# Kernel tuning notes

Measured on AMD Instinct MI355X. Metric: run time of the kernel, lower is better.

Reference implementation:

```python
import jax, jax.numpy as jnp
import numpy as np

TGT, BSZ, E, H = 2048, 4, 1024, 16
HD = E // H


def setup_inputs() -> dict:
    key = jax.random.key(0)
    ks = jax.random.split(key, 9)
    s = 1.0 / np.sqrt(E)
    return {
        "query": jax.random.normal(ks[0], (TGT, BSZ, E), jnp.float32),
        "wq": jax.random.normal(ks[1], (E, E), jnp.float32) * s,
        "bq": jax.random.normal(ks[2], (E,), jnp.float32) * 0.01,
        "wk": jax.random.normal(ks[3], (E, E), jnp.float32) * s,
        "bk": jax.random.normal(ks[4], (E,), jnp.float32) * 0.01,
        "wv": jax.random.normal(ks[5], (E, E), jnp.float32) * s,
        "bv": jax.random.normal(ks[6], (E,), jnp.float32) * 0.01,
        "wo": jax.random.normal(ks[7], (E, E), jnp.float32) * s,
        "bo": jax.random.normal(ks[8], (E,), jnp.float32) * 0.01,
    }


def reference(query, wq, bq, wk, bk, wv, bv, wo, bo):
    tgt_len, bsz, embed_dim = query.shape
    scaling = HD ** (-0.5)
    # self-attention: q,k,v all projected from query (torch Linear: x @ W.T + b)
    q = (query @ wq.T + bq) * scaling
    k = query @ wk.T + bk
    v = query @ wv.T + bv
    # [T, B, E] -> [B, H, T, HD]
    def split_heads(x):
        return x.reshape(tgt_len, bsz, H, HD).transpose(1, 2, 0, 3)
    qh, kh, vh = split_heads(q), split_heads(k), split_heads(v)
    # attention scores [B, H, Tq, Tk]
    scores = jnp.einsum("bhqd,bhkd->bhqk", qh, kh)
    attn = jax.nn.softmax(scores, axis=-1)
    ctx = jnp.einsum("bhqk,bhkd->bhqd", attn, vh)  # [B, H, T, HD]
    ctx = ctx.transpose(2, 0, 1, 3).reshape(tgt_len, bsz, embed_dim)
    out = ctx @ wo.T + bo
    # need_weights=True default: average attn weights over heads [B, Tq, Tk]
    avg_attn = attn.mean(axis=1)
    return out, avg_attn
```

## Files before the change

### kernel.cpp

```cpp
#include <hip/hip_runtime.h>
#include <cstdint>
#include <cstddef>

typedef _Float16 f16;
typedef f16   f16x4 __attribute__((ext_vector_type(4)));
typedef f16   f16x8 __attribute__((ext_vector_type(8)));
typedef float f32x4 __attribute__((ext_vector_type(4)));

#define MFMA16x32(a, b, c) __builtin_amdgcn_mfma_f32_16x16x32_f16((a), (b), (c), 0, 0, 0)
#define MFMA16x16(a, b, c) __builtin_amdgcn_mfma_f32_16x16x16f16((a), (b), (c), 0, 0, 0)

__device__ __forceinline__ void gload_lds16(const void* g, void* l) {
    __builtin_amdgcn_global_load_lds(
        (const __attribute__((address_space(1))) unsigned int*)g,
        (__attribute__((address_space(3))) unsigned int*)l, 16, 0, 0);
}

__global__ void cvt_f32_f16(const float* __restrict__ in, f16* __restrict__ out, int n8) {
    int i = blockIdx.x * blockDim.x + threadIdx.x;
    if (i >= n8) return;
    const float4 a = ((const float4*)in)[i * 2];
    const float4 b = ((const float4*)in)[i * 2 + 1];
    f16x8 o;
    o[0] = (f16)a.x; o[1] = (f16)a.y; o[2] = (f16)a.z; o[3] = (f16)a.w;
    o[4] = (f16)b.x; o[5] = (f16)b.y; o[6] = (f16)b.z; o[7] = (f16)b.w;
    *(f16x8*)(out + (size_t)i * 8) = o;
}

__global__ __launch_bounds__(256, 3)
void gemm_qkv(const f16* __restrict__ A, const f16* __restrict__ B,
              const float* __restrict__ bq, const float* __restrict__ bk,
              const float* __restrict__ bv,
              f16* __restrict__ q_sp, f16* __restrict__ k_sp, f16* __restrict__ v_sp)
{
    __shared__ f16 Al[128 * 32];
    __shared__ f16 Bl[128 * 32];
    const int tid = threadIdx.x, lane = tid & 63, w = tid >> 6;
    const int wm = w >> 1, wn = w & 1;
    const int m0 = blockIdx.y * 128, n0 = blockIdx.x * 128;
    const int l15 = lane & 15, lh = lane >> 4;

    f32x4 acc[4][4] = {};

    const int c0 = w, c1 = w + 4;
    const int srow0 = c0 * 16 + (lane >> 2);
    const int srow1 = c1 * 16 + (lane >> 2);
    const int scol = (lane & 3) * 8;

    for (int k0 = 0; k0 < 1024; k0 += 32) {
        gload_lds16(A + (size_t)(m0 + srow0) * 1024 + k0 + scol, &Al[c0 * 512]);
        gload_lds16(A + (size_t)(m0 + srow1) * 1024 + k0 + scol, &Al[c1 * 512]);
        gload_lds16(B + (size_t)(n0 + srow0) * 1024 + k0 + scol, &Bl[c0 * 512]);
        gload_lds16(B + (size_t)(n0 + srow1) * 1024 + k0 + scol, &Bl[c1 * 512]);
        __syncthreads();
        f16x8 af[4], bf[4];
        #pragma unroll
        for (int i = 0; i < 4; ++i) {
            af[i] = *(const f16x8*)&Al[(wm * 64 + i * 16 + l15) * 32 + lh * 8];
            bf[i] = *(const f16x8*)&Bl[(wn * 64 + i * 16 + l15) * 32 + lh * 8];
        }
        #pragma unroll
        for (int i = 0; i < 4; ++i)
            #pragma unroll
            for (int j = 0; j < 4; ++j)
                acc[i][j] = MFMA16x32(af[i], bf[j], acc[i][j]);
        __syncthreads();
    }

    const int seg = n0 >> 10;
    const float* bias = (seg == 0) ? bq : (seg == 1) ? bk : bv;
    f16* dst = (seg == 0) ? q_sp : (seg == 1) ? k_sp : v_sp;
    const float scale = (seg == 0) ? 0.18033688011112042f : 1.0f;

    #pragma unroll
    for (int j = 0; j < 4; ++j) {
        const int n = n0 + wn * 64 + j * 16 + l15;
        const int e = n & 1023, hh = e >> 6, d = e & 63;
        const float bsv = bias[e];
        #pragma unroll
        for (int i = 0; i < 4; ++i) {
            #pragma unroll
            for (int r = 0; r < 4; ++r) {
                const int m = m0 + wm * 64 + i * 16 + lh * 4 + r;
                const int t = m >> 2, bb = m & 3;
                dst[((size_t)(bb * 16 + hh) * 2048 + t) * 64 + d] =
                    (f16)((acc[i][j][r] + bsv) * scale);
            }
        }
    }
}

__global__ __launch_bounds__(256)
void vpack(const f16* __restrict__ v_sp, f16* __restrict__ vf_) {
    __shared__ f16 L[16 * 64];
    const int nt = blockIdx.x, bh = blockIdx.y;
    const int tid = threadIdx.x;
    const f16* src = v_sp + ((size_t)bh * 2048 + nt * 16) * 64;
    if (tid < 128)
        *(f16x8*)&L[tid * 8] = *(const f16x8*)&src[tid * 8];
    __syncthreads();
    const int lane = tid >> 2, dt = tid & 3;
    const int l15 = lane & 15, lh = lane >> 4;
    f16x4 o;
    #pragma unroll
    for (int r = 0; r < 4; ++r) o[r] = L[(lh * 4 + r) * 64 + dt * 16 + l15];
    *(f16x4*)&vf_[((size_t)bh * 128 + nt) * 1024 + tid * 4] = o;
}

__global__ __launch_bounds__(512, 1)
void attn_kernel(const f16* __restrict__ q_s, const f16* __restrict__ k_s,
                 const f16* __restrict__ v_f, f16* __restrict__ ctx,
                 float* __restrict__ avg_out)
{
    __shared__ float Oacc[2][2][1024];
    __shared__ float sumL[8][2][16];

    const int tid = threadIdx.x;
    const int lane = tid & 63;
    const int w = tid >> 6;
    const int b = blockIdx.y;
    const int t0 = blockIdx.x * 32;
    const int l15 = lane & 15, lh = lane >> 4;

    f16x4 avgv0[16] = {}, avgv1[16] = {};

    {
        float* Oz = &Oacc[0][0][0];
        #pragma unroll
        for (int jj = 0; jj < 8; ++jj) Oz[tid + jj * 512] = 0.f;
    }
    __syncthreads();

    for (int h = 0; h < 16; ++h) {
        const f16* Qh  = q_s + ((size_t)(b * 16 + h) * 2048 + t0) * 64;
        const f16* Kh  = k_s + (size_t)(b * 16 + h) * 2048 * 64 + (size_t)w * 256 * 64;
        const f16* Vfh = v_f + (size_t)(b * 16 + h) * 131072 + (size_t)w * 16 * 1024;

        const f16x8 qa0 = *(const f16x8*)(Qh + l15 * 64 + lh * 8);
        const f16x8 qa1 = *(const f16x8*)(Qh + l15 * 64 + 32 + lh * 8);
        const f16x8 qb0 = *(const f16x8*)(Qh + (16 + l15) * 64 + lh * 8);
        const f16x8 qb1 = *(const f16x8*)(Qh + (16 + l15) * 64 + 32 + lh * 8);

        f16x4 tA[16], tB[16];
        float rsA = 0.f, rsB = 0.f;
        #pragma unroll
        for (int nt = 0; nt < 16; ++nt) {
            const f16* kp = Kh + (size_t)(nt * 16 + l15) * 64 + lh * 8;
            const f16x8 kf0 = *(const f16x8*)(kp);
            const f16x8 kf1 = *(const f16x8*)(kp + 32);
            f32x4 sA = {0.f, 0.f, 0.f, 0.f}, sB = {0.f, 0.f, 0.f, 0.f};
            sA = MFMA16x32(kf0, qa0, sA); sA = MFMA16x32(kf1, qa1, sA);
            sB = MFMA16x32(kf0, qb0, sB); sB = MFMA16x32(kf1, qb1, sB);
            f16x4 ta, tb;
            #pragma unroll
            for (int r = 0; r < 4; ++r) {
                const float eA = __builtin_amdgcn_exp2f(sA[r]);
                const float eB = __builtin_amdgcn_exp2f(sB[r]);
                rsA += eA; rsB += eB;
                ta[r] = (f16)eA; tb[r] = (f16)eB;
            }
            tA[nt] = ta; tB[nt] = tb;
        }
        rsA += __shfl_xor(rsA, 16); rsA += __shfl_xor(rsA, 32);
        rsB += __shfl_xor(rsB, 16); rsB += __shfl_xor(rsB, 32);
        if (lane < 16) { sumL[w][0][lane] = rsA; sumL[w][1][lane] = rsB; }
        __syncthreads();

        {
            float* Oz = &Oacc[(h + 1) & 1][0][0];
            #pragma unroll
            for (int jj = 0; jj < 4; ++jj) Oz[tid + jj * 512] = 0.f;
        }

        float totA = 0.f, totB = 0.f;
        #pragma unroll
        for (int ww = 0; ww < 8; ++ww) {
            totA += sumL[ww][0][l15];
            totB += sumL[ww][1][l15];
        }
        const f16 hiA = (f16)(1.f / totA), hiB = (f16)(1.f / totB);
        f16x4 hvA; hvA[0] = hiA; hvA[1] = hiA; hvA[2] = hiA; hvA[3] = hiA;
        f16x4 hvB; hvB[0] = hiB; hvB[1] = hiB; hvB[2] = hiB; hvB[3] = hiB;

        f32x4 a0 = {}, a1 = {}, a2 = {}, a3 = {};
        f32x4 b0 = {}, b1 = {}, b2 = {}, b3 = {};
        #pragma unroll
        for (int nt = 0; nt < 16; ++nt) {
            const f16x4 tnA = tA[nt] * hvA;
            const f16x4 tnB = tB[nt] * hvB;
            avgv0[nt] += tnA;
            avgv1[nt] += tnB;
            const f16* vp = Vfh + nt * 1024 + lane * 16;
            const f16x8 vab = *(const f16x8*)(vp);
            const f16x8 vcd = *(const f16x8*)(vp + 8);
            const f16x4 va = __builtin_shufflevector(vab, vab, 0, 1, 2, 3);
            const f16x4 vb = __builtin_shufflevector(vab, vab, 4, 5, 6, 7);
            const f16x4 vc = __builtin_shufflevector(vcd, vcd, 0, 1, 2, 3);
            const f16x4 vd = __builtin_shufflevector(vcd, vcd, 4, 5, 6, 7);
            a0 = MFMA16x16(tnA, va, a0); a1 = MFMA16x16(tnA, vb, a1);
            a2 = MFMA16x16(tnA, vc, a2); a3 = MFMA16x16(tnA, vd, a3);
            b0 = MFMA16x16(tnB, va, b0); b1 = MFMA16x16(tnB, vb, b1);
            b2 = MFMA16x16(tnB, vc, b2); b3 = MFMA16x16(tnB, vd, b3);
        }
        float* OA = &Oacc[h & 1][0][0];
        float* OB = &Oacc[h & 1][1][0];
        #pragma unroll
        for (int r = 0; r < 4; ++r) {
            const int rowb = (lh * 4 + r) * 64;
            atomicAdd(&OA[rowb +      l15], a0[r]);
            atomicAdd(&OA[rowb + 16 + l15], a1[r]);
            atomicAdd(&OA[rowb + 32 + l15], a2[r]);
            atomicAdd(&OA[rowb + 48 + l15], a3[r]);
            atomicAdd(&OB[rowb +      l15], b0[r]);
            atomicAdd(&OB[rowb + 16 + l15], b1[r]);
            atomicAdd(&OB[rowb + 32 + l15], b2[r]);
            atomicAdd(&OB[rowb + 48 + l15], b3[r]);
        }
        __syncthreads();

        #pragma unroll
        for (int jj = 0; jj < 4; ++jj) {
            const int idx = tid + jj * 512;
            const int g = idx >> 10, rem = idx & 1023;
            const int q = rem >> 6, d = rem & 63;
            ctx[((size_t)(t0 + g * 16 + q) * 4 + b) * 1024 + h * 64 + d] =
                (f16)Oacc[h & 1][g][rem];
        }
    }

    const float s16 = 1.f / 16.f;
    float* ao0 = avg_out + ((size_t)b * 2048 + t0 + l15) * 2048 + w * 256 + lh * 4;
    float* ao1 = avg_out + ((size_t)b * 2048 + t0 + 16 + l15) * 2048 + w * 256 + lh * 4;
    #pragma unroll
    for (int nt = 0; nt < 16; ++nt) {
        float4 v0, v1;
        v0.x = (float)avgv0[nt][0] * s16; v0.y = (float)avgv0[nt][1] * s16;
        v0.z = (float)avgv0[nt][2] * s16; v0.w = (float)avgv0[nt][3] * s16;
        v1.x = (float)avgv1[nt][0] * s16; v1.y = (float)avgv1[nt][1] * s16;
        v1.z = (float)avgv1[nt][2] * s16; v1.w = (float)avgv1[nt][3] * s16;
        *(float4*)(ao0 + nt * 16) = v0;
        *(float4*)(ao1 + nt * 16) = v1;
    }
}

__global__ __launch_bounds__(256, 3)
void gemm_out(const f16* __restrict__ A, const f16* __restrict__ B,
              const float* __restrict__ bo, float* __restrict__ out)
{
    __shared__ f16 Al[128 * 32];
    __shared__ f16 Bl[128 * 32];
    const int tid = threadIdx.x, lane = tid & 63, w = tid >> 6;
    const int wm = w >> 1, wn = w & 1;
    const int m0 = blockIdx.y * 128, n0 = blockIdx.x * 128;
    const int l15 = lane & 15, lh = lane >> 4;

    f32x4 acc[4][4] = {};
    const int c0 = w, c1 = w + 4;
    const int srow0 = c0 * 16 + (lane >> 2);
    const int srow1 = c1 * 16 + (lane >> 2);
    const int scol = (lane & 3) * 8;

    for (int k0 = 0; k0 < 1024; k0 += 32) {
        gload_lds16(A + (size_t)(m0 + srow0) * 1024 + k0 + scol, &Al[c0 * 512]);
        gload_lds16(A + (size_t)(m0 + srow1) * 1024 + k0 + scol, &Al[c1 * 512]);
        gload_lds16(B + (size_t)(n0 + srow0) * 1024 + k0 + scol, &Bl[c0 * 512]);
        gload_lds16(B + (size_t)(n0 + srow1) * 1024 + k0 + scol, &Bl[c1 * 512]);
        __syncthreads();
        f16x8 af[4], bf[4];
        #pragma unroll
        for (int i = 0; i < 4; ++i) {
            af[i] = *(const f16x8*)&Al[(wm * 64 + i * 16 + l15) * 32 + lh * 8];
            bf[i] = *(const f16x8*)&Bl[(wn * 64 + i * 16 + l15) * 32 + lh * 8];
        }
        #pragma unroll
        for (int i = 0; i < 4; ++i)
            #pragma unroll
            for (int j = 0; j < 4; ++j)
                acc[i][j] = MFMA16x32(af[i], bf[j], acc[i][j]);
        __syncthreads();
    }

    #pragma unroll
    for (int j = 0; j < 4; ++j) {
        const int n = n0 + wn * 64 + j * 16 + l15;
        const float bsv = bo[n];
        #pragma unroll
        for (int i = 0; i < 4; ++i) {
            #pragma unroll
            for (int r = 0; r < 4; ++r) {
                const int m = m0 + wm * 64 + i * 16 + lh * 4 + r;
                out[(size_t)m * 1024 + n] = acc[i][j][r] + bsv;
            }
        }
    }
}

extern "C" void kernel_launch(void* const* d_in, const int* in_sizes, int n_in,
                              void* d_out, int out_size, void* d_ws, size_t ws_size,
                              hipStream_t stream) {
    const float* query = (const float*)d_in[0];
    const float* wq = (const float*)d_in[1];
    const float* bq = (const float*)d_in[2];
    const float* wk = (const float*)d_in[3];
    const float* bk = (const float*)d_in[4];
    const float* wv = (const float*)d_in[5];
    const float* bv = (const float*)d_in[6];
    const float* wo = (const float*)d_in[7];
    const float* bo = (const float*)d_in[8];
    float* out = (float*)d_out;

    f16* wsh  = (f16*)d_ws;
    f16* Xb   = wsh;
    f16* Wqkv = wsh + (8u << 20);
    f16* Wo   = wsh + (11u << 20);
    f16* q_sp = wsh + (12u << 20);
    f16* k_sp = wsh + (20u << 20);
    f16* v_sp = wsh + (28u << 20);
    f16* v_f  = wsh + (36u << 20);
    f16* ctx  = Xb;

    cvt_f32_f16<<<4096, 256, 0, stream>>>(query, Xb, 1048576);
    cvt_f32_f16<<<512, 256, 0, stream>>>(wq, Wqkv, 131072);
    cvt_f32_f16<<<512, 256, 0, stream>>>(wk, Wqkv + (1u << 20), 131072);
    cvt_f32_f16<<<512, 256, 0, stream>>>(wv, Wqkv + (2u << 20), 131072);
    cvt_f32_f16<<<512, 256, 0, stream>>>(wo, Wo, 131072);

    gemm_qkv<<<dim3(24, 64), 256, 0, stream>>>(Xb, Wqkv, bq, bk, bv, q_sp, k_sp, v_sp);
    vpack<<<dim3(128, 64), 256, 0, stream>>>(v_sp, v_f);
    attn_kernel<<<dim3(64, 4), 512, 0, stream>>>(q_sp, k_sp, v_f, ctx,
                                                 out + 8388608 );
    gemm_out<<<dim3(8, 64), 256, 0, stream>>>(ctx, Wo, bo, out);
}
```

Measured before the change: 724.4 us.

## Split attention heads across two grid slices and reduce averaged weights separately

The attention grid grows a z dimension of 2, and each block now handles 8 heads instead of 16, which doubles the block count from 256 to 512. This fills more of the GPU's compute units. The launch bound changes to allow 2 blocks per CU. Each slice's partial sum of head-averaged attention weights is written separately: one slice writes to an f16 scratch buffer, the other writes f32 straight into the output. A new avg_reduce kernel then adds the two and scales by 1/16. The cost is an extra pass reading and writing the 64MB averaged-weights tensor, plus possible register pressure from the tighter occupancy bound.

```diff
diff --git a/kernel.cpp b/kernel.cpp
--- a/kernel.cpp
+++ b/kernel.cpp
@@ -25,6 +25,21 @@
     o[0] = (f16)a.x; o[1] = (f16)a.y; o[2] = (f16)a.z; o[3] = (f16)a.w;
     o[4] = (f16)b.x; o[5] = (f16)b.y; o[6] = (f16)b.z; o[7] = (f16)b.w;
     *(f16x8*)(out + (size_t)i * 8) = o;
+}
+
+__global__ void avg_reduce(const f16* __restrict__ s0, float* __restrict__ out, int n8) {
+    int i = blockIdx.x * blockDim.x + threadIdx.x;
+    if (i >= n8) return;
+    const f16x8 s = *(const f16x8*)(s0 + (size_t)i * 8);
+    float4 a = ((const float4*)out)[i * 2];
+    float4 b = ((const float4*)out)[i * 2 + 1];
+    const float k = 1.f / 16.f;
+    a.x = (a.x + (float)s[0]) * k; a.y = (a.y + (float)s[1]) * k;
+    a.z = (a.z + (float)s[2]) * k; a.w = (a.w + (float)s[3]) * k;
+    b.x = (b.x + (float)s[4]) * k; b.y = (b.y + (float)s[5]) * k;
+    b.z = (b.z + (float)s[6]) * k; b.w = (b.w + (float)s[7]) * k;
+    ((float4*)out)[i * 2] = a;
+    ((float4*)out)[i * 2 + 1] = b;
 }
 
 __global__ __launch_bounds__(256, 3)
@@ -107,10 +122,10 @@
     *(f16x4*)&vf_[((size_t)bh * 128 + nt) * 1024 + tid * 4] = o;
 }
 
-__global__ __launch_bounds__(512, 1)
+__global__ __launch_bounds__(512, 2)
 void attn_kernel(const f16* __restrict__ q_s, const f16* __restrict__ k_s,
                  const f16* __restrict__ v_f, f16* __restrict__ ctx,
-                 float* __restrict__ avg_out)
+                 float* __restrict__ avg_out, f16* __restrict__ pavg)
 {
     __shared__ float Oacc[2][2][1024];
     __shared__ float sumL[8][2][16];
@@ -119,6 +134,7 @@
     const int lane = tid & 63;
     const int w = tid >> 6;
     const int b = blockIdx.y;
+    const int hz = blockIdx.z;
     const int t0 = blockIdx.x * 32;
     const int l15 = lane & 15, lh = lane >> 4;
 
@@ -131,7 +147,8 @@
     }
     __syncthreads();
 
-    for (int h = 0; h < 16; ++h) {
+    for (int i = 0; i < 8; ++i) {
+        const int h = hz * 8 + i;
         const f16* Qh  = q_s + ((size_t)(b * 16 + h) * 2048 + t0) * 64;
         const f16* Kh  = k_s + (size_t)(b * 16 + h) * 2048 * 64 + (size_t)w * 256 * 64;
         const f16* Vfh = v_f + (size_t)(b * 16 + h) * 131072 + (size_t)w * 16 * 1024;
@@ -167,7 +184,7 @@
         __syncthreads();
 
         {
-            float* Oz = &Oacc[(h + 1) & 1][0][0];
+            float* Oz = &Oacc[(i + 1) & 1][0][0];
             #pragma unroll
             for (int jj = 0; jj < 4; ++jj) Oz[tid + jj * 512] = 0.f;
         }
@@ -202,8 +219,8 @@
             b0 = MFMA16x16(tnB, va, b0); b1 = MFMA16x16(tnB, vb, b1);
             b2 = MFMA16x16(tnB, vc, b2); b3 = MFMA16x16(tnB, vd, b3);
         }
-        float* OA = &Oacc[h & 1][0][0];
-        float* OB = &Oacc[h & 1][1][0];
+        float* OA = &Oacc[i & 1][0][0];
+        float* OB = &Oacc[i & 1][1][0];
         #pragma unroll
         for (int r = 0; r < 4; ++r) {
             const int rowb = (lh * 4 + r) * 64;
@@ -224,22 +241,31 @@
             const int g = idx >> 10, rem = idx & 1023;
             const int q = rem >> 6, d = rem & 63;
             ctx[((size_t)(t0 + g * 16 + q) * 4 + b) * 1024 + h * 64 + d] =
-                (f16)Oacc[h & 1][g][rem];
-        }
-    }
-
-    const float s16 = 1.f / 16.f;
-    float* ao0 = avg_out + ((size_t)b * 2048 + t0 + l15) * 2048 + w * 256 + lh * 4;
-    float* ao1 = avg_out + ((size_t)b * 2048 + t0 + 16 + l15) * 2048 + w * 256 + lh * 4;
-    #pragma unroll
-    for (int nt = 0; nt < 16; ++nt) {
-        float4 v0, v1;
-        v0.x = (float)avgv0[nt][0] * s16; v0.y = (float)avgv0[nt][1] * s16;
-        v0.z = (float)avgv0[nt][2] * s16; v0.w = (float)avgv0[nt][3] * s16;
-        v1.x = (float)avgv1[nt][0] * s16; v1.y = (float)avgv1[nt][1] * s16;
-        v1.z = (float)avgv1[nt][2] * s16; v1.w = (float)avgv1[nt][3] * s16;
-        *(float4*)(ao0 + nt * 16) = v0;
-        *(float4*)(ao1 + nt * 16) = v1;
+                (f16)Oacc[i & 1][g][rem];
+        }
+    }
+
+    if (hz == 0) {
+        f16* ao0 = pavg + ((size_t)b * 2048 + t0 + l15) * 2048 + w * 256 + lh * 4;
+        f16* ao1 = pavg + ((size_t)b * 2048 + t0 + 16 + l15) * 2048 + w * 256 + lh * 4;
+        #pragma unroll
+        for (int nt = 0; nt < 16; ++nt) {
+            *(f16x4*)(ao0 + nt * 16) = avgv0[nt];
+            *(f16x4*)(ao1 + nt * 16) = avgv1[nt];
+        }
+    } else {
+        float* ao0 = avg_out + ((size_t)b * 2048 + t0 + l15) * 2048 + w * 256 + lh * 4;
+        float* ao1 = avg_out + ((size_t)b * 2048 + t0 + 16 + l15) * 2048 + w * 256 + lh * 4;
+        #pragma unroll
+        for (int nt = 0; nt < 16; ++nt) {
+            float4 v0, v1;
+            v0.x = (float)avgv0[nt][0]; v0.y = (float)avgv0[nt][1];
+            v0.z = (float)avgv0[nt][2]; v0.w = (float)avgv0[nt][3];
+            v1.x = (float)avgv1[nt][0]; v1.y = (float)avgv1[nt][1];
+            v1.z = (float)avgv1[nt][2]; v1.w = (float)avgv1[nt][3];
+            *(float4*)(ao0 + nt * 16) = v0;
+            *(float4*)(ao1 + nt * 16) = v1;
+        }
     }
 }
 
@@ -317,6 +343,7 @@
     f16* k_sp = wsh + (20u << 20);
     f16* v_sp = wsh + (28u << 20);
     f16* v_f  = wsh + (36u << 20);
+    f16* pavg = wsh + (44u << 20);
     f16* ctx  = Xb;
 
     cvt_f32_f16<<<4096, 256, 0, stream>>>(query, Xb, 1048576);
@@ -327,7 +354,8 @@
 
     gemm_qkv<<<dim3(24, 64), 256, 0, stream>>>(Xb, Wqkv, bq, bk, bv, q_sp, k_sp, v_sp);
     vpack<<<dim3(128, 64), 256, 0, stream>>>(v_sp, v_f);
-    attn_kernel<<<dim3(64, 4), 512, 0, stream>>>(q_sp, k_sp, v_f, ctx,
-                                                 out + 8388608 );
+    attn_kernel<<<dim3(64, 4, 2), 512, 0, stream>>>(q_sp, k_sp, v_f, ctx,
+                                                    out + 8388608 , pavg);
+    avg_reduce<<<8192, 256, 0, stream>>>(pavg, out + 8388608, 2097152);
     gemm_out<<<dim3(8, 64), 256, 0, stream>>>(ctx, Wo, bo, out);
 }
```

Result: slower. 775.8 us (+7.1%).
